# Optimization experiments

Hardware: AMD Instinct MI355X
Metric: run time of the kernel (lower is better)

The kernel has to match this reference:

```python
import jax, jax.numpy as jnp
from jax import lax
import numpy as np

D_STATE = 16
D_CONV = 4
GROUPS = 4
TOKEN = 8


def group_norm(x, w, b, groups, eps=1e-5):
    # x: [B, C, H, W]; torch GroupNorm semantics
    B, C, H, W = x.shape
    xg = x.reshape(B, groups, C // groups, H, W)
    mu = xg.mean(axis=(2, 3, 4), keepdims=True)
    var = ((xg - mu) ** 2).mean(axis=(2, 3, 4), keepdims=True)
    xg = (xg - mu) / jnp.sqrt(var + eps)
    return xg.reshape(B, C, H, W) * w[None, :, None, None] + b[None, :, None, None]


def mamba_fwd(x, in_w, conv_w, conv_b, xproj_w, dt_w, dt_b, A_log, D, out_w):
    # x: [B, L, d_model]. Faithful mamba_ssm Mamba forward (no biases on in/out proj).
    Bsz, L, _ = x.shape
    d_inner = in_w.shape[0] // 2
    dt_rank = dt_w.shape[1]
    xz = x @ in_w.T                                   # [B, L, 2*d_inner]
    xi, z = jnp.split(xz, 2, axis=-1)
    # causal depthwise conv1d (kernel D_CONV) + SiLU
    xc = lax.conv_general_dilated(
        xi.transpose(0, 2, 1), conv_w, window_strides=(1,),
        padding=[(D_CONV - 1, 0)], dimension_numbers=("NCH", "OIH", "NCH"),
        feature_group_count=d_inner)
    xc = jax.nn.silu(xc + conv_b[None, :, None]).transpose(0, 2, 1)  # [B, L, d_inner]
    xdb = xc @ xproj_w.T                               # [B, L, dt_rank + 2*d_state]
    dt, Bm, Cm = jnp.split(xdb, [dt_rank, dt_rank + D_STATE], axis=-1)
    dt = jax.nn.softplus(dt @ dt_w.T + dt_b)           # [B, L, d_inner]
    A = -jnp.exp(A_log)                                # [d_inner, d_state]
    dA = jnp.exp(dt[..., None] * A)                    # [B, L, d_inner, d_state]
    dBx = dt[..., None] * Bm[:, :, None, :] * xc[..., None]

    def step(h, inp):
        dA_t, dBx_t, C_t = inp                         # [B,di,ds],[B,di,ds],[B,ds]
        h = dA_t * h + dBx_t
        y = jnp.einsum('bds,bs->bd', h, C_t)
        return h, y

    h0 = jnp.zeros((Bsz, d_inner, D_STATE), dtype=x.dtype)
    _, ys = lax.scan(step, h0, (dA.transpose(1, 0, 2, 3),
                                dBx.transpose(1, 0, 2, 3),
                                Cm.transpose(1, 0, 2)))
    y = ys.transpose(1, 0, 2) + xc * D                 # skip term D*x
    y = y * jax.nn.silu(z)
    return y @ out_w.T


def setup_inputs() -> dict:
    key = jax.random.key(0)
    ks = iter(jax.random.split(key, 48))

    def rn(shape, s=0.02):
        return jax.random.normal(next(ks), shape, dtype=jnp.float32) * s

    B, C, H, W = 4, 64, 64, 64
    inp = {"x": jax.random.normal(next(ks), (B, C, H, W), dtype=jnp.float32)}

    def mamba_params(prefix, d_model):
        d_inner = 2 * d_model
        dt_rank = -(-d_model // 16)
        inp[prefix + "_in_w"] = rn((2 * d_inner, d_model))
        inp[prefix + "_conv_w"] = rn((d_inner, 1, D_CONV))
        inp[prefix + "_conv_b"] = rn((d_inner,))
        inp[prefix + "_xproj_w"] = rn((dt_rank + 2 * D_STATE, d_inner))
        inp[prefix + "_dt_w"] = rn((d_inner, dt_rank))
        inp[prefix + "_dt_b"] = rn((d_inner,)) + 0.5
        inp[prefix + "_A_log"] = jnp.log(jnp.tile(jnp.arange(1, D_STATE + 1, dtype=jnp.float32), (d_inner, 1)))
        inp[prefix + "_D"] = jnp.ones((d_inner,), jnp.float32)
        inp[prefix + "_out_w"] = rn((d_model, d_inner))

    mamba_params("spa", C)
    mamba_params("spe", -(-C // TOKEN))  # group_channel_num = ceil(64/8) = 8
    inp["spa_gn_w"] = jnp.ones((C,), jnp.float32)
    inp["spa_gn_b"] = jnp.zeros((C,), jnp.float32)
    inp["spe_gn_w"] = jnp.ones((C,), jnp.float32)
    inp["spe_gn_b"] = jnp.zeros((C,), jnp.float32)
    inp["att_w"] = jnp.full((2,), 0.5, jnp.float32)
    return inp


def reference(x,
              spa_in_w, spa_conv_w, spa_conv_b, spa_xproj_w, spa_dt_w, spa_dt_b,
              spa_A_log, spa_D, spa_out_w,
              spe_in_w, spe_conv_w, spe_conv_b, spe_xproj_w, spe_dt_w, spe_dt_b,
              spe_A_log, spe_D, spe_out_w,
              spa_gn_w, spa_gn_b, spe_gn_w, spe_gn_b, att_w):
    B, C, H, W = x.shape
    gcn = -(-C // TOKEN)  # C == TOKEN*gcn here, so no padding path is taken

    # --- SpaMamba: flatten all pixels into one sequence [1, B*H*W, C] ---
    xs = x.transpose(0, 2, 3, 1).reshape(1, -1, C)
    ys = mamba_fwd(xs, spa_in_w, spa_conv_w, spa_conv_b, spa_xproj_w,
                   spa_dt_w, spa_dt_b, spa_A_log, spa_D, spa_out_w)
    ys = ys.reshape(B, H, W, C).transpose(0, 3, 1, 2)
    spa = jax.nn.silu(group_norm(ys, spa_gn_w, spa_gn_b, GROUPS)) + x

    # --- SpeMamba: per-pixel spectral tokens [B*H*W, TOKEN, gcn] ---
    xe = x.transpose(0, 2, 3, 1).reshape(B * H * W, TOKEN, gcn)
    ye = mamba_fwd(xe, spe_in_w, spe_conv_w, spe_conv_b, spe_xproj_w,
                   spe_dt_w, spe_dt_b, spe_A_log, spe_D, spe_out_w)
    ye = ye.reshape(B, H, W, C).transpose(0, 3, 1, 2)
    spe = x + jax.nn.silu(group_norm(ye, spe_gn_w, spe_gn_b, GROUPS))

    w = jax.nn.softmax(att_w)
    return spa * w[0] + spe * w[1] + x
```

## Files before the change

kernel.cpp:

```cpp
#include <hip/hip_runtime.h>

__device__ __forceinline__ float siluf(float x){ return x / (1.f + __expf(-x)); }
__device__ __forceinline__ float softplusf(float x){
    return fmaxf(x, 0.f) + __logf(1.f + __expf(-fabsf(x)));
}
#if __has_builtin(__builtin_amdgcn_exp2f)
__device__ __forceinline__ float fexp2(float x){ return __builtin_amdgcn_exp2f(x); }
#else
__device__ __forceinline__ float fexp2(float x){ return exp2f(x); }
#endif

__global__ void __launch_bounds__(256) k_xpose(const float* __restrict__ x, float* __restrict__ xs){
    __shared__ float t[64][65];
    int blk = blockIdx.x;
    int b = blk >> 6;
    int hw0 = (blk & 63) << 6;
    int tid = threadIdx.x;
    if (blk == 0 && tid < 192) xs[tid] = 0.f;
    const float* xb = x + b*262144 + hw0;
    #pragma unroll
    for (int it = 0; it < 16; ++it){
        int idx = it*256 + tid;
        t[idx>>6][idx&63] = xb[(idx>>6)*4096 + (idx&63)];
    }
    __syncthreads();
    float* xsb = xs + 192 + (size_t)(b*4096 + hw0)*64;
    #pragma unroll
    for (int it = 0; it < 16; ++it){
        int idx = it*256 + tid;
        xsb[(idx>>6)*64 + (idx&63)] = t[idx&63][idx>>6];
    }
}

__global__ void __launch_bounds__(256) k_inproj_conv(const float* __restrict__ xs,
        const float* __restrict__ in_w, const float* __restrict__ cw, const float* __restrict__ cb,
        float* __restrict__ xc, float* __restrict__ zb){
    int tid = threadIdx.x;
    int l0 = blockIdx.x * 8;
    float wr[64];
    const float4* w4 = (const float4*)(in_w + tid*64);
    #pragma unroll
    for (int k = 0; k < 16; ++k){
        float4 v = w4[k];
        wr[4*k]=v.x; wr[4*k+1]=v.y; wr[4*k+2]=v.z; wr[4*k+3]=v.w;
    }
    if (tid < 128){
        float acc[11];
        #pragma unroll
        for (int r = 0; r < 11; ++r) acc[r] = 0.f;
        const float4* xr = ((const float4*)xs) + (size_t)l0*16;
        #pragma unroll
        for (int k = 0; k < 16; ++k){
            #pragma unroll
            for (int r = 0; r < 11; ++r){
                float4 v = xr[r*16 + k];
                acc[r] = fmaf(v.x, wr[4*k],   acc[r]);
                acc[r] = fmaf(v.y, wr[4*k+1], acc[r]);
                acc[r] = fmaf(v.z, wr[4*k+2], acc[r]);
                acc[r] = fmaf(v.w, wr[4*k+3], acc[r]);
            }
        }
        float cw0 = cw[tid*4+0], cw1 = cw[tid*4+1], cw2 = cw[tid*4+2], cw3 = cw[tid*4+3];
        float cbd = cb[tid];
        #pragma unroll
        for (int r = 0; r < 8; ++r){
            float a = fmaf(cw0, acc[r],   cbd);
            a = fmaf(cw1, acc[r+1], a);
            a = fmaf(cw2, acc[r+2], a);
            a = fmaf(cw3, acc[r+3], a);
            xc[(size_t)(l0+r)*128 + tid] = siluf(a);
        }
    } else {
        float acc[8];
        #pragma unroll
        for (int r = 0; r < 8; ++r) acc[r] = 0.f;
        const float4* xr = ((const float4*)(xs + 192)) + (size_t)l0*16;
        #pragma unroll
        for (int k = 0; k < 16; ++k){
            #pragma unroll
            for (int r = 0; r < 8; ++r){
                float4 v = xr[r*16 + k];
                acc[r] = fmaf(v.x, wr[4*k],   acc[r]);
                acc[r] = fmaf(v.y, wr[4*k+1], acc[r]);
                acc[r] = fmaf(v.z, wr[4*k+2], acc[r]);
                acc[r] = fmaf(v.w, wr[4*k+3], acc[r]);
            }
        }
        int dz = tid - 128;
        #pragma unroll
        for (int r = 0; r < 8; ++r) zb[(size_t)(l0+r)*128 + dz] = acc[r];
    }
}

#define XE_  0
#define XCL_ 1216
#define BCL_ 3904
#define DTV_ 8640
#define SPG_ 8768
__global__ void __launch_bounds__(256) k_p1_spe(
        const float* __restrict__ xc, const float* __restrict__ xpw, const float* __restrict__ dtw,
        const float* __restrict__ dtb, const float* __restrict__ A_log,
        float* __restrict__ Pb, float* __restrict__ Qb,
        const float* __restrict__ x,
        const float* __restrict__ ein_w, const float* __restrict__ ecw, const float* __restrict__ ecb,
        const float* __restrict__ expw, const float* __restrict__ edtw, const float* __restrict__ edtb,
        const float* __restrict__ eA_log, const float* __restrict__ eDv, const float* __restrict__ eow,
        float* __restrict__ ye, float* __restrict__ sp)
{
    __shared__ float smem[8800];
    const int tid = threadIdx.x;
    if (blockIdx.x >= 1024){
        float* sxc = smem;
        float* sbm = smem + 4096;
        float* dtr = smem + 4608;
        const int ch = blockIdx.x - 1024;
        {
            const float4* src = (const float4*)(xc + (size_t)ch*4096);
            float4* dst = (float4*)sxc;
            #pragma unroll
            for (int u = 0; u < 4; ++u) dst[u*256 + tid] = src[u*256 + tid];
        }
        __syncthreads();
        {
            int j = tid & 63, tg = tid >> 6;
            if (j < 20){
                const float4* w4  = (const float4*)(xpw + j*128);
                const float4* xc4 = (const float4*)sxc + tg*256;
                float acc[8];
                #pragma unroll
                for (int r = 0; r < 8; ++r) acc[r] = 0.f;
                #pragma unroll 8
                for (int k = 0; k < 32; ++k){
                    float4 w = w4[k];
                    #pragma unroll
                    for (int r = 0; r < 8; ++r){
                        float4 v = xc4[r*32 + k];
                        acc[r] = fmaf(v.x, w.x, acc[r]);
                        acc[r] = fmaf(v.y, w.y, acc[r]);
                        acc[r] = fmaf(v.z, w.z, acc[r]);
                        acc[r] = fmaf(v.w, w.w, acc[r]);
                    }
                }
                if (j < 4){
                    #pragma unroll
                    for (int r = 0; r < 8; ++r) dtr[(tg*8+r)*4 + j] = acc[r];
                } else {
                    #pragma unroll
                    for (int r = 0; r < 8; ++r) sbm[(tg*8+r)*16 + (j-4)] = acc[r];
                }
            }
        }
        __syncthreads();
        const int d  = tid & 127;
        const int sh = tid >> 7;
        float A8[8];
        {
            const float4* al4 = (const float4*)(A_log + d*16 + sh*8);
            float4 v0 = al4[0], v1 = al4[1];
            A8[0]=-__expf(v0.x)*1.44269504f; A8[1]=-__expf(v0.y)*1.44269504f;
            A8[2]=-__expf(v0.z)*1.44269504f; A8[3]=-__expf(v0.w)*1.44269504f;
            A8[4]=-__expf(v1.x)*1.44269504f; A8[5]=-__expf(v1.y)*1.44269504f;
            A8[6]=-__expf(v1.z)*1.44269504f; A8[7]=-__expf(v1.w)*1.44269504f;
        }
        float4 dw = *(const float4*)(dtw + d*4);
        float dbd = dtb[d];
        float P[8], Q[8];
        #pragma unroll
        for (int s = 0; s < 8; ++s){ P[s] = 1.f; Q[s] = 0.f; }
        #pragma unroll 4
        for (int i = 0; i < 32; ++i){
            float4 dt4 = *(const float4*)(dtr + i*4);
            float dv = dbd;
            dv = fmaf(dt4.x, dw.x, dv);
            dv = fmaf(dt4.y, dw.y, dv);
            dv = fmaf(dt4.z, dw.z, dv);
            dv = fmaf(dt4.w, dw.w, dv);
            float dt = softplusf(dv);
            float db = dt * sxc[i*128 + d];
            const float4* bmr = (const float4*)(sbm + i*16 + sh*8);
            float4 b0 = bmr[0], b1 = bmr[1];
            float bv[8] = {b0.x,b0.y,b0.z,b0.w,b1.x,b1.y,b1.z,b1.w};
            #pragma unroll
            for (int s = 0; s < 8; ++s){
                float a = fexp2(dt*A8[s]);
                P[s] *= a;
                Q[s] = fmaf(a, Q[s], db*bv[s]);
            }
        }
        float* Pp = Pb + (size_t)ch*2048 + d*16 + sh*8;
        float* Qp = Qb + (size_t)ch*2048 + d*16 + sh*8;
        ((float4*)Pp)[0] = make_float4(P[0],P[1],P[2],P[3]);
        ((float4*)Pp)[1] = make_float4(P[4],P[5],P[6],P[7]);
        ((float4*)Qp)[0] = make_float4(Q[0],Q[1],Q[2],Q[3]);
        ((float4*)Qp)[1] = make_float4(Q[4],Q[5],Q[6],Q[7]);
    } else {
        const int pix = tid >> 4;
        const int d   = tid & 15;
        const int eb  = blockIdx.x;
        const int p0  = eb * 16;
        const int b   = p0 >> 12;
        const int hw0 = p0 & 4095;

        const float* xb = x + b*262144 + hw0;
        #pragma unroll
        for (int it = 0; it < 4; ++it){
            int idx = it*256 + tid;
            smem[XE_ + (idx&15)*76 + (idx>>4)] = xb[(idx>>4)*4096 + (idx&15)];
        }
        __syncthreads();

        float wi[8], wz[8];
        #pragma unroll
        for (int g = 0; g < 8; ++g){ wi[g] = ein_w[d*8+g]; wz[g] = ein_w[(16+d)*8+g]; }
        float xi[8], zz[8];
        {
            const float4* xe4 = (const float4*)(smem + XE_ + pix*76);
            #pragma unroll
            for (int t = 0; t < 8; ++t){
                float4 a = xe4[t*2], bq = xe4[t*2+1];
                float xv8[8] = {a.x,a.y,a.z,a.w,bq.x,bq.y,bq.z,bq.w};
                float ai = 0.f, az = 0.f;
                #pragma unroll
                for (int g = 0; g < 8; ++g){
                    ai = fmaf(xv8[g], wi[g], ai);
                    az = fmaf(xv8[g], wz[g], az);
                }
                xi[t] = ai; zz[t] = az;
            }
        }
        float c0 = ecw[d*4+0], c1 = ecw[d*4+1], c2 = ecw[d*4+2], c3 = ecw[d*4+3];
        float cbd = ecb[d];
        float xcr[8];
        #pragma unroll
        for (int t = 0; t < 8; ++t){
            float a = fmaf(c3, xi[t], cbd);
            if (t >= 1) a = fmaf(c2, xi[t-1], a);
            if (t >= 2) a = fmaf(c1, xi[t-2], a);
            if (t >= 3) a = fmaf(c0, xi[t-3], a);
            xcr[t] = siluf(a);
            smem[XCL_ + pix*168 + t*20 + d] = xcr[t];
        }
        __syncthreads();

        {
            const int row = tid >> 1;
            const int jh  = tid & 1;
            const int px2 = row >> 3;
            const int t2  = row & 7;
            const float4* xr = (const float4*)(smem + XCL_ + px2*168 + t2*20);
            float4 r0 = xr[0], r1 = xr[1], r2 = xr[2], r3 = xr[3];
            float xv[16] = {r0.x,r0.y,r0.z,r0.w, r1.x,r1.y,r1.z,r1.w,
                            r2.x,r2.y,r2.z,r2.w, r3.x,r3.y,r3.z,r3.w};
            float accd = 0.f;
            #pragma unroll
            for (int k = 0; k < 16; ++k) accd = fmaf(xv[k], expw[k], accd);
            const float* wbase = expw + (1 + jh*16)*16;
            float outv[16];
            #pragma unroll
            for (int s = 0; s < 16; ++s){
                const float* wr = wbase + s*16;
                float a = 0.f;
                #pragma unroll
                for (int k = 0; k < 16; ++k) a = fmaf(xv[k], wr[k], a);
                outv[s] = a;
            }
            float* dstb = smem + BCL_ + px2*296 + t2*36 + jh*16;
            #pragma unroll
            for (int s = 0; s < 16; ++s) dstb[s] = outv[s];
            if (jh == 0) smem[DTV_ + px2*8 + t2] = accd;
        }
        __syncthreads();

        float A16[16];
        #pragma unroll
        for (int s = 0; s < 16; ++s) A16[s] = -__expf(eA_log[d*16+s]) * 1.44269504f;
        float dwd = edtw[d], dbd = edtb[d], Dd = eDv[d];
        float h[16];
        #pragma unroll
        for (int s = 0; s < 16; ++s) h[s] = 0.f;
        #pragma unroll
        for (int t = 0; t < 8; ++t){
            float dtd = softplusf(fmaf(smem[DTV_ + pix*8 + t], dwd, dbd));
            float db = dtd * xcr[t];
            const float4* bc4 = (const float4*)(smem + BCL_ + pix*296 + t*36);
            float4 b0 = bc4[0], b1 = bc4[1], b2 = bc4[2], b3 = bc4[3];
            float4 cc0 = bc4[4], cc1 = bc4[5], cc2 = bc4[6], cc3 = bc4[7];
            float bv[16] = {b0.x,b0.y,b0.z,b0.w, b1.x,b1.y,b1.z,b1.w,
                            b2.x,b2.y,b2.z,b2.w, b3.x,b3.y,b3.z,b3.w};
            float cv[16] = {cc0.x,cc0.y,cc0.z,cc0.w, cc1.x,cc1.y,cc1.z,cc1.w,
                            cc2.x,cc2.y,cc2.z,cc2.w, cc3.x,cc3.y,cc3.z,cc3.w};
            float yp = 0.f;
            #pragma unroll
            for (int s = 0; s < 16; ++s){
                float a = fexp2(dtd*A16[s]);
                h[s] = fmaf(a, h[s], db*bv[s]);
                yp = fmaf(h[s], cv[s], yp);
            }
            smem[pix*168 + t*20 + d] = (yp + xcr[t]*Dd) * siluf(zz[t]);
        }
        __syncthreads();

        int tt = d >> 1, m0 = (d & 1)*4;
        const float4* y4 = (const float4*)(smem + pix*168 + tt*20);
        float4 y0 = y4[0], y1 = y4[1], y2 = y4[2], y3 = y4[3];
        float ylr[16] = {y0.x,y0.y,y0.z,y0.w, y1.x,y1.y,y1.z,y1.w,
                         y2.x,y2.y,y2.z,y2.w, y3.x,y3.y,y3.z,y3.w};
        float acc[4];
        #pragma unroll
        for (int mm = 0; mm < 4; ++mm){
            const float* wr = eow + (m0+mm)*16;
            float a = 0.f;
            #pragma unroll
            for (int k = 0; k < 16; ++k) a = fmaf(ylr[k], wr[k], a);
            acc[mm] = a;
        }
        float4 o; o.x=acc[0]; o.y=acc[1]; o.z=acc[2]; o.w=acc[3];
        *(float4*)(ye + (size_t)(p0+pix)*64 + tt*8 + m0) = o;

        float s  = acc[0]+acc[1]+acc[2]+acc[3];
        float ss = acc[0]*acc[0]+acc[1]*acc[1]+acc[2]*acc[2]+acc[3]*acc[3];
        s += __shfl_xor(s,1);  ss += __shfl_xor(ss,1);
        s += __shfl_xor(s,2);  ss += __shfl_xor(ss,2);
        s += __shfl_xor(s,16); ss += __shfl_xor(ss,16);
        s += __shfl_xor(s,32); ss += __shfl_xor(ss,32);
        int lane = tid & 63, wv = tid >> 6;
        if ((lane & 51) == 0){ smem[SPG_ + wv*4 + ((lane>>2)&3)] = s; smem[SPG_ + 16 + wv*4 + ((lane>>2)&3)] = ss; }
        __syncthreads();
        if (tid < 4){
            int blk = eb & 255;
            float S  = smem[SPG_+0*4+tid]+smem[SPG_+1*4+tid]+smem[SPG_+2*4+tid]+smem[SPG_+3*4+tid];
            float SS = smem[SPG_+16+0*4+tid]+smem[SPG_+16+1*4+tid]+smem[SPG_+16+2*4+tid]+smem[SPG_+16+3*4+tid];
            float* dst = sp + (size_t)(((4 + b)*4 + tid)*512 + blk*2);
            dst[0] = S; dst[1] = SS;
        }
    }
}

__global__ void __launch_bounds__(256) k_scan_p2a(const float* __restrict__ Pb,
        const float* __restrict__ Qb, float* __restrict__ Ps, float* __restrict__ Qs){
    int g = blockIdx.x*256 + threadIdx.x;
    int sup = g >> 11;
    int lane = g & 2047;
    float P = 1.f, Q = 0.f;
    for (int i = 0; i < 32; i += 8){
        float p[8], q[8];
        #pragma unroll
        for (int u = 0; u < 8; ++u){
            p[u] = Pb[(size_t)(sup*32+i+u)*2048 + lane];
            q[u] = Qb[(size_t)(sup*32+i+u)*2048 + lane];
        }
        #pragma unroll
        for (int u = 0; u < 8; ++u){
            P = p[u]*P;
            Q = fmaf(p[u], Q, q[u]);
        }
    }
    Ps[g] = P; Qs[g] = Q;
}

__global__ void __launch_bounds__(256) k_scan_p2c(const float* __restrict__ Pb,
        const float* __restrict__ Qb, const float* __restrict__ Ps,
        const float* __restrict__ Qs, float* __restrict__ Hs){
    int g = blockIdx.x*256 + threadIdx.x;
    int sup = g >> 11;
    int lane = g & 2047;
    float h = 0.f;
    for (int u = 0; u < sup; ++u){
        float p = Ps[u*2048 + lane];
        float q = Qs[u*2048 + lane];
        h = fmaf(p, h, q);
    }
    for (int i = 0; i < 32; i += 8){
        float p[8], q[8];
        #pragma unroll
        for (int u = 0; u < 8; ++u){
            p[u] = Pb[(size_t)(sup*32+i+u)*2048 + lane];
            q[u] = Qb[(size_t)(sup*32+i+u)*2048 + lane];
        }
        #pragma unroll
        for (int u = 0; u < 8; ++u){
            Hs[(size_t)(sup*32+i+u)*2048 + lane] = h;
            h = fmaf(p[u], h, q[u]);
        }
    }
}

__global__ void __launch_bounds__(256) k_scan_p3(const float* __restrict__ xc,
        const float* __restrict__ zb, const float* __restrict__ xpw, const float* __restrict__ dtw,
        const float* __restrict__ dtb, const float* __restrict__ A_log, const float* __restrict__ Dv,
        const float* __restrict__ Hs, const float* __restrict__ ow,
        float* __restrict__ ys, float* __restrict__ sp){
    __shared__ float sxc[32*128];
    __shared__ float ypl[2][32*128];
    __shared__ float sbm[32*16];
    __shared__ float scm[32*16];
    __shared__ __align__(16) float dtr[32][4];
    __shared__ float pgs[2][2][4];
    const int tid = threadIdx.x;
    const int ch = blockIdx.x;
    {
        const float4* src = (const float4*)(xc + (size_t)ch*4096);
        float4* dst = (float4*)sxc;
        #pragma unroll
        for (int u = 0; u < 4; ++u) dst[u*256 + tid] = src[u*256 + tid];
    }
    __syncthreads();
    {
        int j = tid & 63, tg = tid >> 6;
        if (j < 36){
            const float4* w4  = (const float4*)(xpw + j*128);
            const float4* xc4 = (const float4*)sxc + tg*256;
            float acc[8];
            #pragma unroll
            for (int r = 0; r < 8; ++r) acc[r] = 0.f;
            #pragma unroll 8
            for (int k = 0; k < 32; ++k){
                float4 w = w4[k];
                #pragma unroll
                for (int r = 0; r < 8; ++r){
                    float4 v = xc4[r*32 + k];
                    acc[r] = fmaf(v.x, w.x, acc[r]);
                    acc[r] = fmaf(v.y, w.y, acc[r]);
                    acc[r] = fmaf(v.z, w.z, acc[r]);
                    acc[r] = fmaf(v.w, w.w, acc[r]);
                }
            }
            if (j < 4){
                #pragma unroll
                for (int r = 0; r < 8; ++r) dtr[tg*8+r][j] = acc[r];
            } else if (j < 20){
                #pragma unroll
                for (int r = 0; r < 8; ++r) sbm[(tg*8+r)*16 + (j-4)] = acc[r];
            } else {
                #pragma unroll
                for (int r = 0; r < 8; ++r) scm[(tg*8+r)*16 + (j-20)] = acc[r];
            }
        }
    }
    __syncthreads();
    const int d  = tid & 127;
    const int sh = tid >> 7;
    float A8[8], h[8];
    {
        const float4* al4 = (const float4*)(A_log + d*16 + sh*8);
        float4 v0 = al4[0], v1 = al4[1];
        A8[0]=-__expf(v0.x)*1.44269504f; A8[1]=-__expf(v0.y)*1.44269504f;
        A8[2]=-__expf(v0.z)*1.44269504f; A8[3]=-__expf(v0.w)*1.44269504f;
        A8[4]=-__expf(v1.x)*1.44269504f; A8[5]=-__expf(v1.y)*1.44269504f;
        A8[6]=-__expf(v1.z)*1.44269504f; A8[7]=-__expf(v1.w)*1.44269504f;
        const float4* h4 = (const float4*)(Hs + (size_t)ch*2048 + d*16 + sh*8);
        float4 h0 = h4[0], h1 = h4[1];
        h[0]=h0.x; h[1]=h0.y; h[2]=h0.z; h[3]=h0.w;
        h[4]=h1.x; h[5]=h1.y; h[6]=h1.z; h[7]=h1.w;
    }
    float4 dw = *(const float4*)(dtw + d*4);
    float dbd = dtb[d];
    #pragma unroll 4
    for (int i = 0; i < 32; ++i){
        float4 dt4 = *(const float4*)dtr[i];
        float dv = dbd;
        dv = fmaf(dt4.x, dw.x, dv);
        dv = fmaf(dt4.y, dw.y, dv);
        dv = fmaf(dt4.z, dw.z, dv);
        dv = fmaf(dt4.w, dw.w, dv);
        float dt = softplusf(dv);
        float db = dt * sxc[i*128 + d];
        const float4* bmr = (const float4*)(sbm + i*16 + sh*8);
        const float4* cmr = (const float4*)(scm + i*16 + sh*8);
        float4 b0 = bmr[0], b1 = bmr[1];
        float4 c0 = cmr[0], c1 = cmr[1];
        float bv[8] = {b0.x,b0.y,b0.z,b0.w,b1.x,b1.y,b1.z,b1.w};
        float cv[8] = {c0.x,c0.y,c0.z,c0.w,c1.x,c1.y,c1.z,c1.w};
        float yp = 0.f;
        #pragma unroll
        for (int s = 0; s < 8; ++s){
            float a = fexp2(dt*A8[s]);
            h[s] = fmaf(a, h[s], db*bv[s]);
            yp = fmaf(h[s], cv[s], yp);
        }
        ypl[sh][i*128 + d] = yp;
    }
    __syncthreads();
    #pragma unroll
    for (int it = 0; it < 16; ++it){
        int idx = it*256 + tid;
        float yp = ypl[0][idx] + ypl[1][idx];
        float xcd = sxc[idx];
        float zv = zb[(size_t)ch*4096 + idx];
        ypl[0][idx] = (yp + xcd*Dv[idx & 127]) * siluf(zv);
    }
    __syncthreads();
    {
        int c  = tid & 63;
        int kh = (tid >> 6) & 1;
        int rg = tid >> 7;
        float wr[64];
        const float4* w4o = (const float4*)(ow + c*128 + kh*64);
        #pragma unroll
        for (int k = 0; k < 16; ++k){
            float4 v = w4o[k];
            wr[4*k]=v.x; wr[4*k+1]=v.y; wr[4*k+2]=v.z; wr[4*k+3]=v.w;
        }
        float acc[16];
        #pragma unroll
        for (int r = 0; r < 16; ++r) acc[r] = 0.f;
        const float4* y4 = (const float4*)(ypl[0] + rg*16*128 + kh*64);
        #pragma unroll
        for (int k = 0; k < 16; ++k){
            #pragma unroll
            for (int r = 0; r < 16; ++r){
                float4 v = y4[r*32 + k];
                acc[r] = fmaf(v.x, wr[4*k],   acc[r]);
                acc[r] = fmaf(v.y, wr[4*k+1], acc[r]);
                acc[r] = fmaf(v.z, wr[4*k+2], acc[r]);
                acc[r] = fmaf(v.w, wr[4*k+3], acc[r]);
            }
        }
        float* part = ypl[1];
        if (kh == 1){
            #pragma unroll
            for (int r = 0; r < 16; ++r) part[(rg*16+r)*64 + c] = acc[r];
        }
        __syncthreads();
        if (kh == 0){
            float s = 0.f, ss = 0.f;
            #pragma unroll
            for (int r = 0; r < 16; ++r){
                float v = acc[r] + part[(rg*16+r)*64 + c];
                ys[(size_t)(ch*32 + rg*16 + r)*64 + c] = v;
                s += v; ss += v*v;
            }
            s += __shfl_xor(s,1); ss += __shfl_xor(ss,1);
            s += __shfl_xor(s,2); ss += __shfl_xor(ss,2);
            s += __shfl_xor(s,4); ss += __shfl_xor(ss,4);
            s += __shfl_xor(s,8); ss += __shfl_xor(ss,8);
            if ((c & 15) == 0){ pgs[0][rg][c>>4] = s; pgs[1][rg][c>>4] = ss; }
        }
        __syncthreads();
        if (tid < 4){
            int b = ch >> 7, blk = ch & 127;
            float S  = pgs[0][0][tid] + pgs[0][1][tid];
            float SS = pgs[1][0][tid] + pgs[1][1][tid];
            float* dst = sp + (size_t)((b*4 + tid)*512 + blk*2);
            dst[0] = S; dst[1] = SS;
        }
    }
}

__global__ void __launch_bounds__(256) k_final(const float* __restrict__ x,
        const float* __restrict__ ys, const float* __restrict__ ye,
        const float* __restrict__ sp,
        const float* __restrict__ gsw, const float* __restrict__ gsb,
        const float* __restrict__ gew, const float* __restrict__ geb,
        const float* __restrict__ attw, float* __restrict__ out){
    __shared__ float st[16];
    __shared__ float tys[32][65];
    __shared__ float tye[32][65];
    int tid = threadIdx.x;
    int b   = blockIdx.x >> 7;
    int hw0 = (blockIdx.x & 127) << 5;
    {
        int combo = tid >> 5;
        int j = tid & 31;
        int t = combo >> 2, g = combo & 3;
        float s = 0.f, ss = 0.f;
        if (t == 0){
            const float4* bp = (const float4*)(sp + (size_t)(b*4 + g)*512 + j*8);
            #pragma unroll
            for (int k = 0; k < 2; ++k){ float4 v = bp[k]; s += v.x+v.z; ss += v.y+v.w; }
        } else {
            const float4* bp = (const float4*)(sp + (size_t)((4+b)*4 + g)*512 + j*16);
            #pragma unroll
            for (int k = 0; k < 4; ++k){ float4 v = bp[k]; s += v.x+v.z; ss += v.y+v.w; }
        }
        s += __shfl_xor(s,1);  ss += __shfl_xor(ss,1);
        s += __shfl_xor(s,2);  ss += __shfl_xor(ss,2);
        s += __shfl_xor(s,4);  ss += __shfl_xor(ss,4);
        s += __shfl_xor(s,8);  ss += __shfl_xor(ss,8);
        s += __shfl_xor(s,16); ss += __shfl_xor(ss,16);
        if (j == 0){
            float m = s * (1.f/65536.f);
            float v = ss * (1.f/65536.f) - m*m;
            st[combo*2]   = m;
            st[combo*2+1] = rsqrtf(v + 1e-5f);
        }
    }
    const float* ysb = ys + ((size_t)(b*4096 + hw0))*64;
    const float* yeb = ye + ((size_t)(b*4096 + hw0))*64;
    #pragma unroll
    for (int it = 0; it < 8; ++it){
        int idx = it*256 + tid;
        tys[idx>>6][idx&63] = ysb[idx];
        tye[idx>>6][idx&63] = yeb[idx];
    }
    __syncthreads();
    float a0 = attw[0], a1 = attw[1];
    float mx = fmaxf(a0, a1);
    float e0 = __expf(a0-mx), e1 = __expf(a1-mx);
    float inv = 1.f/(e0+e1);
    float w0 = e0*inv, w1 = e1*inv;
    #pragma unroll
    for (int it = 0; it < 8; ++it){
        int idx = it*256 + tid;
        int c = idx >> 5, hwi = idx & 31;
        int g = c >> 4;
        size_t gx = ((size_t)(b*64 + c))*4096 + hw0 + hwi;
        float xv = x[gx];
        float ns = (tys[hwi][c] - st[g*2])     * st[g*2+1]     * gsw[c] + gsb[c];
        float ne = (tye[hwi][c] - st[8+g*2])   * st[8+g*2+1]   * gew[c] + geb[c];
        out[gx] = w0*(siluf(ns)+xv) + w1*(xv+siluf(ne)) + xv;
    }
}

#define OFF_XS 0u
#define OFF_XC 1048832u
#define OFF_Z  3145984u
#define OFF_PB 5243136u
#define OFF_QB 6291712u
#define OFF_HS 7340288u
#define OFF_YE 8388864u
#define OFF_PS 9437440u
#define OFF_QS 9470208u
#define OFF_SP 9502976u

extern "C" void kernel_launch(void* const* d_in, const int* in_sizes, int n_in,
                              void* d_out, int out_size, void* d_ws, size_t ws_size,
                              hipStream_t stream) {
    const float* x           = (const float*)d_in[0];
    const float* spa_in_w    = (const float*)d_in[1];
    const float* spa_conv_w  = (const float*)d_in[2];
    const float* spa_conv_b  = (const float*)d_in[3];
    const float* spa_xproj_w = (const float*)d_in[4];
    const float* spa_dt_w    = (const float*)d_in[5];
    const float* spa_dt_b    = (const float*)d_in[6];
    const float* spa_A_log   = (const float*)d_in[7];
    const float* spa_D       = (const float*)d_in[8];
    const float* spa_out_w   = (const float*)d_in[9];
    const float* spe_in_w    = (const float*)d_in[10];
    const float* spe_conv_w  = (const float*)d_in[11];
    const float* spe_conv_b  = (const float*)d_in[12];
    const float* spe_xproj_w = (const float*)d_in[13];
    const float* spe_dt_w    = (const float*)d_in[14];
    const float* spe_dt_b    = (const float*)d_in[15];
    const float* spe_A_log   = (const float*)d_in[16];
    const float* spe_D       = (const float*)d_in[17];
    const float* spe_out_w   = (const float*)d_in[18];
    const float* spa_gn_w    = (const float*)d_in[19];
    const float* spa_gn_b    = (const float*)d_in[20];
    const float* spe_gn_w    = (const float*)d_in[21];
    const float* spe_gn_b    = (const float*)d_in[22];
    const float* att_w       = (const float*)d_in[23];

    float* ws  = (float*)d_ws;
    float* xs  = ws + OFF_XS;
    float* xc  = ws + OFF_XC;
    float* zb  = ws + OFF_Z;
    float* Pb  = ws + OFF_PB;
    float* Qb  = ws + OFF_QB;
    float* Hs  = ws + OFF_HS;
    float* Ps  = ws + OFF_PS;
    float* Qs  = ws + OFF_QS;
    float* sp  = ws + OFF_SP;
    float* ysb = ws + OFF_XS;
    float* yeb = ws + OFF_YE;
    float* out = (float*)d_out;

    k_xpose      <<<256,  256, 0, stream>>>(x, xs);
    k_inproj_conv<<<2048, 256, 0, stream>>>(xs, spa_in_w, spa_conv_w, spa_conv_b, xc, zb);
    k_p1_spe     <<<1536, 256, 0, stream>>>(xc, spa_xproj_w, spa_dt_w, spa_dt_b, spa_A_log,
                                            Pb, Qb,
                                            x, spe_in_w, spe_conv_w, spe_conv_b, spe_xproj_w,
                                            spe_dt_w, spe_dt_b, spe_A_log, spe_D, spe_out_w,
                                            yeb, sp);
    k_scan_p2a   <<<128,  256, 0, stream>>>(Pb, Qb, Ps, Qs);
    k_scan_p2c   <<<128,  256, 0, stream>>>(Pb, Qb, Ps, Qs, Hs);
    k_scan_p3    <<<512,  256, 0, stream>>>(xc, zb, spa_xproj_w, spa_dt_w, spa_dt_b,
                                            spa_A_log, spa_D, Hs, spa_out_w, ysb, sp);
    k_final      <<<512,  256, 0, stream>>>(x, ysb, yeb, sp, spa_gn_w, spa_gn_b,
                                            spe_gn_w, spe_gn_b, att_w, out);
}
```

Measured before the change: 120.2 us.

## Halve scan chunk length and interleave spatial and spectral blocks in phase one

Splits the spatial Mamba scan into 16-token chunks instead of 32. Phase-1 blocks now emit two chunk summaries each, phase-2 scans walk 64 chunks per super-chunk, and phase 3 launches twice as many smaller blocks. The spatial and spectral blocks in the phase-1 kernel are interleaved 1:2 by blockIdx so the two kinds of work mix across CUs. The intent is more parallelism and less serial work per block in phase 3, at the cost of more P/Q/H workspace traffic and more sequential steps in the phase-2 chain.

```diff
diff --git a/kernel.cpp b/kernel.cpp
--- a/kernel.cpp
+++ b/kernel.cpp
@@ -109,11 +109,13 @@
 {
     __shared__ float smem[8800];
     const int tid = threadIdx.x;
-    if (blockIdx.x >= 1024){
+    const int m3 = blockIdx.x % 3;
+    const int q3 = blockIdx.x / 3;
+    if (m3 == 1){
         float* sxc = smem;
         float* sbm = smem + 4096;
         float* dtr = smem + 4608;
-        const int ch = blockIdx.x - 1024;
+        const int ch = q3;
         {
             const float4* src = (const float4*)(xc + (size_t)ch*4096);
             float4* dst = (float4*)sxc;
@@ -164,11 +166,11 @@
         }
         float4 dw = *(const float4*)(dtw + d*4);
         float dbd = dtb[d];
-        float P[8], Q[8];
+        float P[8], Q[8], P1[8], Q1[8];
         #pragma unroll
         for (int s = 0; s < 8; ++s){ P[s] = 1.f; Q[s] = 0.f; }
         #pragma unroll 4
-        for (int i = 0; i < 32; ++i){
+        for (int i = 0; i < 16; ++i){
             float4 dt4 = *(const float4*)(dtr + i*4);
             float dv = dbd;
             dv = fmaf(dt4.x, dw.x, dv);
@@ -187,16 +189,42 @@
                 Q[s] = fmaf(a, Q[s], db*bv[s]);
             }
         }
-        float* Pp = Pb + (size_t)ch*2048 + d*16 + sh*8;
-        float* Qp = Qb + (size_t)ch*2048 + d*16 + sh*8;
-        ((float4*)Pp)[0] = make_float4(P[0],P[1],P[2],P[3]);
-        ((float4*)Pp)[1] = make_float4(P[4],P[5],P[6],P[7]);
-        ((float4*)Qp)[0] = make_float4(Q[0],Q[1],Q[2],Q[3]);
-        ((float4*)Qp)[1] = make_float4(Q[4],Q[5],Q[6],Q[7]);
+        #pragma unroll
+        for (int s = 0; s < 8; ++s){ P1[s] = P[s]; Q1[s] = Q[s]; P[s] = 1.f; Q[s] = 0.f; }
+        #pragma unroll 4
+        for (int i = 16; i < 32; ++i){
+            float4 dt4 = *(const float4*)(dtr + i*4);
+            float dv = dbd;
+            dv = fmaf(dt4.x, dw.x, dv);
+            dv = fmaf(dt4.y, dw.y, dv);
+            dv = fmaf(dt4.z, dw.z, dv);
+            dv = fmaf(dt4.w, dw.w, dv);
+            float dt = softplusf(dv);
+            float db = dt * sxc[i*128 + d];
+            const float4* bmr = (const float4*)(sbm + i*16 + sh*8);
+            float4 b0 = bmr[0], b1 = bmr[1];
+            float bv[8] = {b0.x,b0.y,b0.z,b0.w,b1.x,b1.y,b1.z,b1.w};
+            #pragma unroll
+            for (int s = 0; s < 8; ++s){
+                float a = fexp2(dt*A8[s]);
+                P[s] *= a;
+                Q[s] = fmaf(a, Q[s], db*bv[s]);
+            }
+        }
+        float* Pp = Pb + (size_t)(2*ch)*2048 + d*16 + sh*8;
+        float* Qp = Qb + (size_t)(2*ch)*2048 + d*16 + sh*8;
+        ((float4*)Pp)[0] = make_float4(P1[0],P1[1],P1[2],P1[3]);
+        ((float4*)Pp)[1] = make_float4(P1[4],P1[5],P1[6],P1[7]);
+        ((float4*)Qp)[0] = make_float4(Q1[0],Q1[1],Q1[2],Q1[3]);
+        ((float4*)Qp)[1] = make_float4(Q1[4],Q1[5],Q1[6],Q1[7]);
+        ((float4*)(Pp+2048))[0] = make_float4(P[0],P[1],P[2],P[3]);
+        ((float4*)(Pp+2048))[1] = make_float4(P[4],P[5],P[6],P[7]);
+        ((float4*)(Qp+2048))[0] = make_float4(Q[0],Q[1],Q[2],Q[3]);
+        ((float4*)(Qp+2048))[1] = make_float4(Q[4],Q[5],Q[6],Q[7]);
     } else {
         const int pix = tid >> 4;
         const int d   = tid & 15;
-        const int eb  = blockIdx.x;
+        const int eb  = q3*2 + (m3 >> 1);
         const int p0  = eb * 16;
         const int b   = p0 >> 12;
         const int hw0 = p0 & 4095;
@@ -342,12 +370,12 @@
     int sup = g >> 11;
     int lane = g & 2047;
     float P = 1.f, Q = 0.f;
-    for (int i = 0; i < 32; i += 8){
+    for (int i = 0; i < 64; i += 8){
         float p[8], q[8];
         #pragma unroll
         for (int u = 0; u < 8; ++u){
-            p[u] = Pb[(size_t)(sup*32+i+u)*2048 + lane];
-            q[u] = Qb[(size_t)(sup*32+i+u)*2048 + lane];
+            p[u] = Pb[(size_t)(sup*64+i+u)*2048 + lane];
+            q[u] = Qb[(size_t)(sup*64+i+u)*2048 + lane];
         }
         #pragma unroll
         for (int u = 0; u < 8; ++u){
@@ -370,16 +398,16 @@
         float q = Qs[u*2048 + lane];
         h = fmaf(p, h, q);
     }
-    for (int i = 0; i < 32; i += 8){
+    for (int i = 0; i < 64; i += 8){
         float p[8], q[8];
         #pragma unroll
         for (int u = 0; u < 8; ++u){
-            p[u] = Pb[(size_t)(sup*32+i+u)*2048 + lane];
-            q[u] = Qb[(size_t)(sup*32+i+u)*2048 + lane];
+            p[u] = Pb[(size_t)(sup*64+i+u)*2048 + lane];
+            q[u] = Qb[(size_t)(sup*64+i+u)*2048 + lane];
         }
         #pragma unroll
         for (int u = 0; u < 8; ++u){
-            Hs[(size_t)(sup*32+i+u)*2048 + lane] = h;
+            Hs[(size_t)(sup*64+i+u)*2048 + lane] = h;
             h = fmaf(p[u], h, q[u]);
         }
     }
@@ -390,34 +418,34 @@
         const float* __restrict__ dtb, const float* __restrict__ A_log, const float* __restrict__ Dv,
         const float* __restrict__ Hs, const float* __restrict__ ow,
         float* __restrict__ ys, float* __restrict__ sp){
-    __shared__ float sxc[32*128];
-    __shared__ float ypl[2][32*128];
-    __shared__ float sbm[32*16];
-    __shared__ float scm[32*16];
-    __shared__ __align__(16) float dtr[32][4];
+    __shared__ float sxc[16*128];
+    __shared__ float ypl[2][16*128];
+    __shared__ float sbm[16*16];
+    __shared__ float scm[16*16];
+    __shared__ __align__(16) float dtr[16][4];
     __shared__ float pgs[2][2][4];
     const int tid = threadIdx.x;
     const int ch = blockIdx.x;
     {
-        const float4* src = (const float4*)(xc + (size_t)ch*4096);
+        const float4* src = (const float4*)(xc + (size_t)ch*2048);
         float4* dst = (float4*)sxc;
-        #pragma unroll
-        for (int u = 0; u < 4; ++u) dst[u*256 + tid] = src[u*256 + tid];
+        dst[tid] = src[tid];
+        dst[256 + tid] = src[256 + tid];
     }
     __syncthreads();
     {
         int j = tid & 63, tg = tid >> 6;
         if (j < 36){
             const float4* w4  = (const float4*)(xpw + j*128);
-            const float4* xc4 = (const float4*)sxc + tg*256;
-            float acc[8];
-            #pragma unroll
-            for (int r = 0; r < 8; ++r) acc[r] = 0.f;
+            const float4* xc4 = (const float4*)sxc + tg*128;
+            float acc[4];
+            #pragma unroll
+            for (int r = 0; r < 4; ++r) acc[r] = 0.f;
             #pragma unroll 8
             for (int k = 0; k < 32; ++k){
                 float4 w = w4[k];
                 #pragma unroll
-                for (int r = 0; r < 8; ++r){
+                for (int r = 0; r < 4; ++r){
                     float4 v = xc4[r*32 + k];
                     acc[r] = fmaf(v.x, w.x, acc[r]);
                     acc[r] = fmaf(v.y, w.y, acc[r]);
@@ -427,13 +455,13 @@
             }
             if (j < 4){
                 #pragma unroll
-                for (int r = 0; r < 8; ++r) dtr[tg*8+r][j] = acc[r];
+                for (int r = 0; r < 4; ++r) dtr[tg*4+r][j] = acc[r];
             } else if (j < 20){
                 #pragma unroll
-                for (int r = 0; r < 8; ++r) sbm[(tg*8+r)*16 + (j-4)] = acc[r];
+                for (int r = 0; r < 4; ++r) sbm[(tg*4+r)*16 + (j-4)] = acc[r];
             } else {
                 #pragma unroll
-                for (int r = 0; r < 8; ++r) scm[(tg*8+r)*16 + (j-20)] = acc[r];
+                for (int r = 0; r < 4; ++r) scm[(tg*4+r)*16 + (j-20)] = acc[r];
             }
         }
     }
@@ -456,7 +484,7 @@
     float4 dw = *(const float4*)(dtw + d*4);
     float dbd = dtb[d];
     #pragma unroll 4
-    for (int i = 0; i < 32; ++i){
+    for (int i = 0; i < 16; ++i){
         float4 dt4 = *(const float4*)dtr[i];
         float dv = dbd;
         dv = fmaf(dt4.x, dw.x, dv);
@@ -482,11 +510,11 @@
     }
     __syncthreads();
     #pragma unroll
-    for (int it = 0; it < 16; ++it){
+    for (int it = 0; it < 8; ++it){
         int idx = it*256 + tid;
         float yp = ypl[0][idx] + ypl[1][idx];
         float xcd = sxc[idx];
-        float zv = zb[(size_t)ch*4096 + idx];
+        float zv = zb[(size_t)ch*2048 + idx];
         ypl[0][idx] = (yp + xcd*Dv[idx & 127]) * siluf(zv);
     }
     __syncthreads();
@@ -501,14 +529,14 @@
             float4 v = w4o[k];
             wr[4*k]=v.x; wr[4*k+1]=v.y; wr[4*k+2]=v.z; wr[4*k+3]=v.w;
         }
-        float acc[16];
-        #pragma unroll
-        for (int r = 0; r < 16; ++r) acc[r] = 0.f;
-        const float4* y4 = (const float4*)(ypl[0] + rg*16*128 + kh*64);
+        float acc[8];
+        #pragma unroll
+        for (int r = 0; r < 8; ++r) acc[r] = 0.f;
+        const float4* y4 = (const float4*)(ypl[0] + rg*8*128 + kh*64);
         #pragma unroll
         for (int k = 0; k < 16; ++k){
             #pragma unroll
-            for (int r = 0; r < 16; ++r){
+            for (int r = 0; r < 8; ++r){
                 float4 v = y4[r*32 + k];
                 acc[r] = fmaf(v.x, wr[4*k],   acc[r]);
                 acc[r] = fmaf(v.y, wr[4*k+1], acc[r]);
@@ -519,15 +547,15 @@
         float* part = ypl[1];
         if (kh == 1){
             #pragma unroll
-            for (int r = 0; r < 16; ++r) part[(rg*16+r)*64 + c] = acc[r];
+            for (int r = 0; r < 8; ++r) part[(rg*8+r)*64 + c] = acc[r];
         }
         __syncthreads();
         if (kh == 0){
             float s = 0.f, ss = 0.f;
             #pragma unroll
-            for (int r = 0; r < 16; ++r){
-                float v = acc[r] + part[(rg*16+r)*64 + c];
-                ys[(size_t)(ch*32 + rg*16 + r)*64 + c] = v;
+            for (int r = 0; r < 8; ++r){
+                float v = acc[r] + part[(rg*8+r)*64 + c];
+                ys[(size_t)(ch*16 + rg*8 + r)*64 + c] = v;
                 s += v; ss += v*v;
             }
             s += __shfl_xor(s,1); ss += __shfl_xor(ss,1);
@@ -538,7 +566,7 @@
         }
         __syncthreads();
         if (tid < 4){
-            int b = ch >> 7, blk = ch & 127;
+            int b = ch >> 8, blk = ch & 255;
             float S  = pgs[0][0][tid] + pgs[0][1][tid];
             float SS = pgs[1][0][tid] + pgs[1][1][tid];
             float* dst = sp + (size_t)((b*4 + tid)*512 + blk*2);
@@ -563,16 +591,10 @@
         int combo = tid >> 5;
         int j = tid & 31;
         int t = combo >> 2, g = combo & 3;
+        const float4* bp = (const float4*)(sp + (size_t)(t*16 + b*4 + g)*512 + j*16);
         float s = 0.f, ss = 0.f;
-        if (t == 0){
-            const float4* bp = (const float4*)(sp + (size_t)(b*4 + g)*512 + j*8);
-            #pragma unroll
-            for (int k = 0; k < 2; ++k){ float4 v = bp[k]; s += v.x+v.z; ss += v.y+v.w; }
-        } else {
-            const float4* bp = (const float4*)(sp + (size_t)((4+b)*4 + g)*512 + j*16);
-            #pragma unroll
-            for (int k = 0; k < 4; ++k){ float4 v = bp[k]; s += v.x+v.z; ss += v.y+v.w; }
-        }
+        #pragma unroll
+        for (int k = 0; k < 4; ++k){ float4 v = bp[k]; s += v.x+v.z; ss += v.y+v.w; }
         s += __shfl_xor(s,1);  ss += __shfl_xor(ss,1);
         s += __shfl_xor(s,2);  ss += __shfl_xor(ss,2);
         s += __shfl_xor(s,4);  ss += __shfl_xor(ss,4);
@@ -616,12 +638,12 @@
 #define OFF_XC 1048832u
 #define OFF_Z  3145984u
 #define OFF_PB 5243136u
-#define OFF_QB 6291712u
-#define OFF_HS 7340288u
-#define OFF_YE 8388864u
-#define OFF_PS 9437440u
-#define OFF_QS 9470208u
-#define OFF_SP 9502976u
+#define OFF_QB 7340288u
+#define OFF_HS 9437440u
+#define OFF_YE 11534592u
+#define OFF_PS 12583168u
+#define OFF_QS 12615936u
+#define OFF_SP 12648704u
 
 extern "C" void kernel_launch(void* const* d_in, const int* in_sizes, int n_in,
                               void* d_out, int out_size, void* d_ws, size_t ws_size,
@@ -674,7 +696,7 @@
                                             yeb, sp);
     k_scan_p2a   <<<128,  256, 0, stream>>>(Pb, Qb, Ps, Qs);
     k_scan_p2c   <<<128,  256, 0, stream>>>(Pb, Qb, Ps, Qs, Hs);
-    k_scan_p3    <<<512,  256, 0, stream>>>(xc, zb, spa_xproj_w, spa_dt_w, spa_dt_b,
+    k_scan_p3    <<<1024, 256, 0, stream>>>(xc, zb, spa_xproj_w, spa_dt_w, spa_dt_b,
                                             spa_A_log, spa_D, Hs, spa_out_w, ysb, sp);
     k_final      <<<512,  256, 0, stream>>>(x, ysb, yeb, sp, spa_gn_w, spa_gn_b,
                                             spe_gn_w, spe_gn_b, att_w, out);
```

Result: slower. 132.2 us (+10.0%).
